# Performance work log

Hardware: AMD Instinct MI355X
Metric: run time of the kernel (lower is better)

## Reference

```python
import jax, jax.numpy as jnp
import numpy as np

B, T, D, P = 8, 2048, 768, 1024


def setup_inputs() -> dict:
    key = jax.random.key(0)
    kx, kp = jax.random.split(key)
    x = jax.random.normal(kx, (B, T, D), dtype=jnp.float32)
    prototypes = jax.random.normal(kp, (P, D), dtype=jnp.float32)
    return {"x": x, "prototypes": prototypes}


def reference(x, prototypes):
    # sum((x[...,None,:] - p)**2, -1) without the [B,T,P,D] intermediate)
    x_sq = jnp.sum(x * x, axis=-1, keepdims=True)          # [B,T,1]
    p_sq = jnp.sum(prototypes * prototypes, axis=-1)        # [P]
    cross = jnp.einsum("btd,pd->btp", x, prototypes)       # [B,T,P]
    distances = x_sq + p_sq[None, None, :] - 2.0 * cross    # [B,T,P]
    return distances, prototypes
```

## Files before the change

kernel.cpp:

```cpp
#include <hip/hip_runtime.h>
#include <hip/hip_bf16.h>
#include <stdint.h>

#define M_ROWS 16384
#define N_COLS 1024
#define K_DIM  768

typedef __attribute__((ext_vector_type(8))) short bf16x8;
typedef __attribute__((ext_vector_type(4))) float f32x4;

__device__ __forceinline__ void async_copy16(void* lds, const void* g) {
  __builtin_amdgcn_global_load_lds(
      (const __attribute__((address_space(1))) unsigned int*)g,
      (__attribute__((address_space(3))) unsigned int*)lds,
      16, 0, 0);
}

__device__ __forceinline__ unsigned short f2bf(float f) {
  __hip_bfloat16 h = __float2bfloat16(f);
  return *reinterpret_cast<unsigned short*>(&h);
}

__global__ void prep_rows(const float* __restrict__ src,
                          unsigned short* __restrict__ dstb,
                          float* __restrict__ sq,
                          float* __restrict__ copy_out) {
  const int wid = threadIdx.x >> 6;
  const int lane = threadIdx.x & 63;
  const int row = blockIdx.x * 4 + wid;
  const float4* r = (const float4*)(src + (size_t)row * K_DIM);
  ushort4* rb = (ushort4*)(dstb + (size_t)row * K_DIM);
  float4* cp = copy_out ? (float4*)(copy_out + (size_t)row * K_DIM) : nullptr;
  float acc = 0.f;
#pragma unroll
  for (int i = 0; i < 3; ++i) {
    float4 v = r[i * 64 + lane];
    acc += v.x * v.x + v.y * v.y + v.z * v.z + v.w * v.w;
    ushort4 u;
    u.x = f2bf(v.x); u.y = f2bf(v.y); u.z = f2bf(v.z); u.w = f2bf(v.w);
    rb[i * 64 + lane] = u;
    if (cp) cp[i * 64 + lane] = v;
  }
#pragma unroll
  for (int off = 32; off; off >>= 1) acc += __shfl_down(acc, off);
  if (lane == 0) sq[row] = acc;
}

__global__ void dist_gemm(const __hip_bfloat16* __restrict__ xb,
                          const __hip_bfloat16* __restrict__ pb,
                          const float* __restrict__ xsq,
                          const float* __restrict__ psq,
                          float* __restrict__ out) {
  __shared__ __hip_bfloat16 As[128 * 32];
  __shared__ __hip_bfloat16 Bs[128 * 32];

  const int flat = blockIdx.x;
  const int xcd = flat & 7;
  const int local = flat >> 3;
  const int bm = xcd * 16 + (local >> 3);
  const int bn = local & 7;

  const int tid = threadIdx.x;
  const int wave = tid >> 6;
  const int lane = tid & 63;
  const int wm = wave >> 1;
  const int wn = wave & 1;

  f32x4 acc[4][4];
#pragma unroll
  for (int i = 0; i < 4; ++i)
#pragma unroll
    for (int j = 0; j < 4; ++j) {
      f32x4 z = {0.f, 0.f, 0.f, 0.f};
      acc[i][j] = z;
    }

  const __hip_bfloat16* Ab = xb + (size_t)(bm * 128) * K_DIM;
  const __hip_bfloat16* Bb = pb + (size_t)(bn * 128) * K_DIM;

  const int sr[2] = {tid >> 2, 64 + (tid >> 2)};
  int gofs[2];
#pragma unroll
  for (int c = 0; c < 2; ++c) {
    const int row = sr[c];
    const int g = (tid & 3) ^ ((row >> 1) & 3);
    gofs[c] = row * K_DIM + g * 8;
  }

  const int rA = lane & 15;
  const int ks = lane >> 4;

  for (int k0 = 0; k0 < K_DIM; k0 += 32) {
#pragma unroll
    for (int c = 0; c < 2; ++c) {
      const int lofs = (c * 256 + tid) * 16;
      async_copy16((char*)As + lofs, Ab + gofs[c] + k0);
      async_copy16((char*)Bs + lofs, Bb + gofs[c] + k0);
    }
    __syncthreads();

    bf16x8 a[4], b[4];
#pragma unroll
    for (int i = 0; i < 4; ++i) {
      const int ra = wm * 64 + i * 16 + rA;
      const int rb = wn * 64 + i * 16 + rA;
      a[i] = *(const bf16x8*)((const char*)As + (ra * 64 + ((ks ^ ((ra >> 1) & 3)) * 16)));
      b[i] = *(const bf16x8*)((const char*)Bs + (rb * 64 + ((ks ^ ((rb >> 1) & 3)) * 16)));
    }
#pragma unroll
    for (int i = 0; i < 4; ++i)
#pragma unroll
      for (int j = 0; j < 4; ++j)
        acc[i][j] = __builtin_amdgcn_mfma_f32_16x16x32_bf16(a[i], b[j], acc[i][j], 0, 0, 0);
    __syncthreads();
  }

  const int colf = lane & 15;
  const int rowg = (lane >> 4) * 4;
#pragma unroll
  for (int j = 0; j < 4; ++j) {
    const int col = bn * 128 + wn * 64 + j * 16 + colf;
    const float ps = psq[col];
#pragma unroll
    for (int i = 0; i < 4; ++i) {
      const int rbase = bm * 128 + wm * 64 + i * 16 + rowg;
#pragma unroll
      for (int r = 0; r < 4; ++r) {
        const int row = rbase + r;
        out[(size_t)row * N_COLS + col] = xsq[row] + ps - 2.0f * acc[i][j][r];
      }
    }
  }
}

extern "C" void kernel_launch(void* const* d_in, const int* in_sizes, int n_in,
                              void* d_out, int out_size, void* d_ws, size_t ws_size,
                              hipStream_t stream) {
  const float* x = (const float*)d_in[0];
  const float* p = (const float*)d_in[1];
  float* out = (float*)d_out;
  char* ws = (char*)d_ws;

  float* xsq = (float*)ws;
  float* psq = (float*)(ws + 65536);
  unsigned short* xb = (unsigned short*)(ws + 69632);
  unsigned short* pb = xb + (size_t)M_ROWS * K_DIM;
  float* proto_out = out + (size_t)M_ROWS * N_COLS;

  prep_rows<<<M_ROWS / 4, 256, 0, stream>>>(x, xb, xsq, nullptr);
  prep_rows<<<N_COLS / 4, 256, 0, stream>>>(p, pb, psq, proto_out);

  dist_gemm<<<1024, 256, 0, stream>>>((const __hip_bfloat16*)xb,
                                      (const __hip_bfloat16*)pb,
                                      xsq, psq, out);
}
```

Baseline: 57.41 us.

## Rewrite distance GEMM as 256x256 double-buffered tile with interleaved prefetch

Replaces the 128x128 single-buffered GEMM, which synchronized twice per 32-wide K step, with 256x256 tiles, 8 waves, 64-wide K steps and double-buffered LDS. Loads for the next K tile are split into four quarter stages interleaved between MFMA clusters, with barriers and setprio to overlap memory and compute. The aim is more operand reuse and hiding global load latency. The cost is 128KB of LDS per block and only 256 blocks, which may underfill the GPU and limit occupancy.

```diff
diff --git a/kernel.cpp b/kernel.cpp
--- a/kernel.cpp
+++ b/kernel.cpp
@@ -5,6 +5,7 @@
 #define M_ROWS 16384
 #define N_COLS 1024
 #define K_DIM  768
+#define NKT    12
 
 typedef __attribute__((ext_vector_type(8))) short bf16x8;
 typedef __attribute__((ext_vector_type(4))) float f32x4;
@@ -46,88 +47,159 @@
   if (lane == 0) sq[row] = acc;
 }
 
-__global__ void dist_gemm(const __hip_bfloat16* __restrict__ xb,
-                          const __hip_bfloat16* __restrict__ pb,
-                          const float* __restrict__ xsq,
-                          const float* __restrict__ psq,
-                          float* __restrict__ out) {
-  __shared__ __hip_bfloat16 As[128 * 32];
-  __shared__ __hip_bfloat16 Bs[128 * 32];
+__device__ __forceinline__ bf16x8 ldsfrag(const char* tile, int row, int slot) {
+  return *(const bf16x8*)(tile + row * 128 + (((slot ^ (row & 7)) << 4)));
+}
+
+__global__ __launch_bounds__(512, 2) void dist_gemm(
+    const __hip_bfloat16* __restrict__ xb,
+    const __hip_bfloat16* __restrict__ pb,
+    const float* __restrict__ xsq,
+    const float* __restrict__ psq,
+    float* __restrict__ out) {
+  __shared__ char lds[2][2][32768];
 
   const int flat = blockIdx.x;
   const int xcd = flat & 7;
   const int local = flat >> 3;
-  const int bm = xcd * 16 + (local >> 3);
-  const int bn = local & 7;
+  const int bm = xcd * 8 + (local >> 2);
+  const int bn = local & 3;
 
   const int tid = threadIdx.x;
   const int wave = tid >> 6;
   const int lane = tid & 63;
-  const int wm = wave >> 1;
-  const int wn = wave & 1;
-
-  f32x4 acc[4][4];
-#pragma unroll
-  for (int i = 0; i < 4; ++i)
-#pragma unroll
-    for (int j = 0; j < 4; ++j) {
-      f32x4 z = {0.f, 0.f, 0.f, 0.f};
-      acc[i][j] = z;
-    }
-
-  const __hip_bfloat16* Ab = xb + (size_t)(bm * 128) * K_DIM;
-  const __hip_bfloat16* Bb = pb + (size_t)(bn * 128) * K_DIM;
-
-  const int sr[2] = {tid >> 2, 64 + (tid >> 2)};
-  int gofs[2];
-#pragma unroll
-  for (int c = 0; c < 2; ++c) {
-    const int row = sr[c];
-    const int g = (tid & 3) ^ ((row >> 1) & 3);
-    gofs[c] = row * K_DIM + g * 8;
-  }
-
-  const int rA = lane & 15;
-  const int ks = lane >> 4;
-
-  for (int k0 = 0; k0 < K_DIM; k0 += 32) {
-#pragma unroll
-    for (int c = 0; c < 2; ++c) {
-      const int lofs = (c * 256 + tid) * 16;
-      async_copy16((char*)As + lofs, Ab + gofs[c] + k0);
-      async_copy16((char*)Bs + lofs, Bb + gofs[c] + k0);
-    }
-    __syncthreads();
-
-    bf16x8 a[4], b[4];
-#pragma unroll
-    for (int i = 0; i < 4; ++i) {
-      const int ra = wm * 64 + i * 16 + rA;
-      const int rb = wn * 64 + i * 16 + rA;
-      a[i] = *(const bf16x8*)((const char*)As + (ra * 64 + ((ks ^ ((ra >> 1) & 3)) * 16)));
-      b[i] = *(const bf16x8*)((const char*)Bs + (rb * 64 + ((ks ^ ((rb >> 1) & 3)) * 16)));
-    }
-#pragma unroll
-    for (int i = 0; i < 4; ++i)
-#pragma unroll
-      for (int j = 0; j < 4; ++j)
-        acc[i][j] = __builtin_amdgcn_mfma_f32_16x16x32_bf16(a[i], b[j], acc[i][j], 0, 0, 0);
-    __syncthreads();
-  }
-
-  const int colf = lane & 15;
-  const int rowg = (lane >> 4) * 4;
-#pragma unroll
-  for (int j = 0; j < 4; ++j) {
-    const int col = bn * 128 + wn * 64 + j * 16 + colf;
-    const float ps = psq[col];
-#pragma unroll
-    for (int i = 0; i < 4; ++i) {
-      const int rbase = bm * 128 + wm * 64 + i * 16 + rowg;
+  const int wm = wave >> 2;
+  const int wn = wave & 3;
+  const int rl = lane & 15;
+  const int kq = lane >> 4;
+
+  f32x4 acc[8][4] = {};
+  bf16x8 af[4][2], bfr[4][2];
+
+  const __hip_bfloat16* Abase = xb + (size_t)(bm * 256) * K_DIM;
+  const __hip_bfloat16* Bbase = pb + (size_t)(bn * 256) * K_DIM;
+
+  const int rih = tid >> 3;
+  const int g8 = (((tid & 7) ^ (rih & 7))) * 8;
+
+#define STAGE(base, tile, h, ktile)                                          \
+  do {                                                                       \
+    _Pragma("unroll") for (int c = 0; c < 2; ++c) {                          \
+      async_copy16((tile) + (h) * 16384 + (c * 512 + tid) * 16,              \
+                   (base) + (size_t)((h) * 128 + c * 64 + rih) * K_DIM +     \
+                       (ktile) * 64 + g8);                                   \
+    }                                                                        \
+  } while (0)
+
+  {
+    char* A0 = &lds[0][0][0];
+    char* B0 = &lds[0][1][0];
+    STAGE(Abase, A0, 0, 0);
+    STAGE(Abase, A0, 1, 0);
+    STAGE(Bbase, B0, 0, 0);
+    STAGE(Bbase, B0, 1, 0);
+  }
+  asm volatile("s_waitcnt vmcnt(0)" ::: "memory");
+  asm volatile("s_barrier" ::: "memory");
+
+  for (int kt = 0; kt < NKT; ++kt) {
+    const char* At = &lds[kt & 1][0][0];
+    const char* Bt = &lds[kt & 1][1][0];
+    char* An = &lds[(kt + 1) & 1][0][0];
+    char* Bn = &lds[(kt + 1) & 1][1][0];
+    const bool pf = (kt + 1 < NKT);
+
+#pragma unroll
+    for (int mi = 0; mi < 4; ++mi)
+#pragma unroll
+      for (int kk = 0; kk < 2; ++kk)
+        af[mi][kk] = ldsfrag(At, wm * 128 + mi * 16 + rl, kk * 4 + kq);
+#pragma unroll
+    for (int ni = 0; ni < 2; ++ni)
+#pragma unroll
+      for (int kk = 0; kk < 2; ++kk)
+        bfr[ni][kk] = ldsfrag(Bt, wn * 64 + ni * 16 + rl, kk * 4 + kq);
+    if (pf) STAGE(Abase, An, 0, kt + 1);
+    asm volatile("s_barrier" ::: "memory");
+    __builtin_amdgcn_s_setprio(1);
+#pragma unroll
+    for (int mi = 0; mi < 4; ++mi)
+#pragma unroll
+      for (int ni = 0; ni < 2; ++ni)
+#pragma unroll
+        for (int kk = 0; kk < 2; ++kk)
+          acc[mi][ni] = __builtin_amdgcn_mfma_f32_16x16x32_bf16(
+              af[mi][kk], bfr[ni][kk], acc[mi][ni], 0, 0, 0);
+    __builtin_amdgcn_s_setprio(0);
+    asm volatile("s_barrier" ::: "memory");
+
+#pragma unroll
+    for (int ni = 2; ni < 4; ++ni)
+#pragma unroll
+      for (int kk = 0; kk < 2; ++kk)
+        bfr[ni][kk] = ldsfrag(Bt, wn * 64 + ni * 16 + rl, kk * 4 + kq);
+    if (pf) STAGE(Abase, An, 1, kt + 1);
+    asm volatile("s_barrier" ::: "memory");
+    __builtin_amdgcn_s_setprio(1);
+#pragma unroll
+    for (int mi = 0; mi < 4; ++mi)
+#pragma unroll
+      for (int ni = 0; ni < 2; ++ni)
+#pragma unroll
+        for (int kk = 0; kk < 2; ++kk)
+          acc[mi][2 + ni] = __builtin_amdgcn_mfma_f32_16x16x32_bf16(
+              af[mi][kk], bfr[2 + ni][kk], acc[mi][2 + ni], 0, 0, 0);
+    __builtin_amdgcn_s_setprio(0);
+    asm volatile("s_barrier" ::: "memory");
+
+#pragma unroll
+    for (int mi = 0; mi < 4; ++mi)
+#pragma unroll
+      for (int kk = 0; kk < 2; ++kk)
+        af[mi][kk] = ldsfrag(At, wm * 128 + 64 + mi * 16 + rl, kk * 4 + kq);
+    if (pf) STAGE(Bbase, Bn, 0, kt + 1);
+    asm volatile("s_barrier" ::: "memory");
+    __builtin_amdgcn_s_setprio(1);
+#pragma unroll
+    for (int mi = 0; mi < 4; ++mi)
+#pragma unroll
+      for (int ni = 0; ni < 2; ++ni)
+#pragma unroll
+        for (int kk = 0; kk < 2; ++kk)
+          acc[4 + mi][ni] = __builtin_amdgcn_mfma_f32_16x16x32_bf16(
+              af[mi][kk], bfr[ni][kk], acc[4 + mi][ni], 0, 0, 0);
+    __builtin_amdgcn_s_setprio(0);
+    asm volatile("s_barrier" ::: "memory");
+
+    if (pf) STAGE(Bbase, Bn, 1, kt + 1);
+    asm volatile("s_barrier" ::: "memory");
+    __builtin_amdgcn_s_setprio(1);
+#pragma unroll
+    for (int mi = 0; mi < 4; ++mi)
+#pragma unroll
+      for (int ni = 0; ni < 2; ++ni)
+#pragma unroll
+        for (int kk = 0; kk < 2; ++kk)
+          acc[4 + mi][2 + ni] = __builtin_amdgcn_mfma_f32_16x16x32_bf16(
+              af[mi][kk], bfr[2 + ni][kk], acc[4 + mi][2 + ni], 0, 0, 0);
+    __builtin_amdgcn_s_setprio(0);
+    asm volatile("s_waitcnt vmcnt(0)" ::: "memory");
+    asm volatile("s_barrier" ::: "memory");
+  }
+#undef STAGE
+
+  const int r0 = bm * 256 + wm * 128;
+  const int c0 = bn * 256 + wn * 64;
+#pragma unroll
+  for (int mf = 0; mf < 8; ++mf) {
+#pragma unroll
+    for (int nf = 0; nf < 4; ++nf) {
+      const int col = c0 + nf * 16 + rl;
+      const float ps = psq[col];
 #pragma unroll
       for (int r = 0; r < 4; ++r) {
-        const int row = rbase + r;
-        out[(size_t)row * N_COLS + col] = xsq[row] + ps - 2.0f * acc[i][j][r];
+        const int row = r0 + mf * 16 + kq * 4 + r;
+        out[(size_t)row * N_COLS + col] = xsq[row] + ps - 2.0f * acc[mf][nf][r];
       }
     }
   }
@@ -150,7 +222,7 @@
   prep_rows<<<M_ROWS / 4, 256, 0, stream>>>(x, xb, xsq, nullptr);
   prep_rows<<<N_COLS / 4, 256, 0, stream>>>(p, pb, psq, proto_out);
 
-  dist_gemm<<<1024, 256, 0, stream>>>((const __hip_bfloat16*)xb,
-                                      (const __hip_bfloat16*)pb,
-                                      xsq, psq, out);
-}
+  dist_gemm<<<256, 512, 0, stream>>>((const __hip_bfloat16*)xb,
+                                     (const __hip_bfloat16*)pb,
+                                     xsq, psq, out);
+}
```

Measured after the change: 51.98 us. 1.1x faster.

## Double-buffer LDS with 64-wide K tiles and merge prep kernels

Applied to the files above, without the earlier changes.

The GEMM now stages 64-wide K tiles into two LDS buffers. The next tile's async global-to-LDS copy is issued before computing on the current one, which replaces the load-sync-compute-sync loop with one barrier per iteration. It uses an 8-way XOR swizzle for the wider rows, raises MFMA wave priority during compute, and sets launch bounds for two blocks per CU. The two prep launches are fused into one kernel to save a launch. LDS use rises to 64KB per block, which may limit occupancy.

```diff
diff --git a/kernel.cpp b/kernel.cpp
--- a/kernel.cpp
+++ b/kernel.cpp
@@ -5,6 +5,7 @@
 #define M_ROWS 16384
 #define N_COLS 1024
 #define K_DIM  768
+#define NKT    12
 
 typedef __attribute__((ext_vector_type(8))) short bf16x8;
 typedef __attribute__((ext_vector_type(4))) float f32x4;
@@ -21,16 +22,31 @@
   return *reinterpret_cast<unsigned short*>(&h);
 }
 
-__global__ void prep_rows(const float* __restrict__ src,
-                          unsigned short* __restrict__ dstb,
-                          float* __restrict__ sq,
-                          float* __restrict__ copy_out) {
+__global__ void prep_all(const float* __restrict__ x,
+                         const float* __restrict__ p,
+                         unsigned short* __restrict__ xb,
+                         unsigned short* __restrict__ pbu,
+                         float* __restrict__ xsq,
+                         float* __restrict__ psq,
+                         float* __restrict__ proto_out) {
+  const int b = blockIdx.x;
   const int wid = threadIdx.x >> 6;
   const int lane = threadIdx.x & 63;
-  const int row = blockIdx.x * 4 + wid;
+  const float* src;
+  unsigned short* dst;
+  float* sq;
+  float* cp;
+  int row;
+  if (b < M_ROWS / 4) {
+    row = b * 4 + wid;
+    src = x; dst = xb; sq = xsq; cp = nullptr;
+  } else {
+    row = (b - M_ROWS / 4) * 4 + wid;
+    src = p; dst = pbu; sq = psq; cp = proto_out;
+  }
   const float4* r = (const float4*)(src + (size_t)row * K_DIM);
-  ushort4* rb = (ushort4*)(dstb + (size_t)row * K_DIM);
-  float4* cp = copy_out ? (float4*)(copy_out + (size_t)row * K_DIM) : nullptr;
+  ushort4* rb = (ushort4*)(dst + (size_t)row * K_DIM);
+  float4* cpv = cp ? (float4*)(cp + (size_t)row * K_DIM) : nullptr;
   float acc = 0.f;
 #pragma unroll
   for (int i = 0; i < 3; ++i) {
@@ -39,20 +55,24 @@
     ushort4 u;
     u.x = f2bf(v.x); u.y = f2bf(v.y); u.z = f2bf(v.z); u.w = f2bf(v.w);
     rb[i * 64 + lane] = u;
-    if (cp) cp[i * 64 + lane] = v;
+    if (cpv) cpv[i * 64 + lane] = v;
   }
 #pragma unroll
   for (int off = 32; off; off >>= 1) acc += __shfl_down(acc, off);
   if (lane == 0) sq[row] = acc;
 }
 
-__global__ void dist_gemm(const __hip_bfloat16* __restrict__ xb,
-                          const __hip_bfloat16* __restrict__ pb,
-                          const float* __restrict__ xsq,
-                          const float* __restrict__ psq,
-                          float* __restrict__ out) {
-  __shared__ __hip_bfloat16 As[128 * 32];
-  __shared__ __hip_bfloat16 Bs[128 * 32];
+__device__ __forceinline__ bf16x8 ldsfrag(const char* tile, int row, int slot) {
+  return *(const bf16x8*)(tile + row * 128 + (((slot ^ (row & 7)) << 4)));
+}
+
+__global__ __launch_bounds__(256, 2) void dist_gemm(
+    const __hip_bfloat16* __restrict__ xb,
+    const __hip_bfloat16* __restrict__ pb,
+    const float* __restrict__ xsq,
+    const float* __restrict__ psq,
+    float* __restrict__ out) {
+  __shared__ char lds[2][2][16384];
 
   const int flat = blockIdx.x;
   const int xcd = flat & 7;
@@ -65,69 +85,81 @@
   const int lane = tid & 63;
   const int wm = wave >> 1;
   const int wn = wave & 1;
+  const int rl = lane & 15;
+  const int kq = lane >> 4;
 
-  f32x4 acc[4][4];
+  f32x4 acc[4][4] = {};
+  bf16x8 af[4][2], bfr[4][2];
+
+  const __hip_bfloat16* Abase = xb + (size_t)(bm * 128) * K_DIM;
+  const __hip_bfloat16* Bbase = pb + (size_t)(bn * 128) * K_DIM;
+
+  int gofs[4];
 #pragma unroll
-  for (int i = 0; i < 4; ++i)
-#pragma unroll
-    for (int j = 0; j < 4; ++j) {
-      f32x4 z = {0.f, 0.f, 0.f, 0.f};
-      acc[i][j] = z;
-    }
-
-  const __hip_bfloat16* Ab = xb + (size_t)(bm * 128) * K_DIM;
-  const __hip_bfloat16* Bb = pb + (size_t)(bn * 128) * K_DIM;
-
-  const int sr[2] = {tid >> 2, 64 + (tid >> 2)};
-  int gofs[2];
-#pragma unroll
-  for (int c = 0; c < 2; ++c) {
-    const int row = sr[c];
-    const int g = (tid & 3) ^ ((row >> 1) & 3);
+  for (int c = 0; c < 4; ++c) {
+    const int row = c * 32 + (tid >> 3);
+    const int g = (tid & 7) ^ (row & 7);
     gofs[c] = row * K_DIM + g * 8;
   }
 
-  const int rA = lane & 15;
-  const int ks = lane >> 4;
+#define STAGE(buf, ktile)                                                   \
+  do {                                                                      \
+    _Pragma("unroll") for (int c = 0; c < 4; ++c) {                         \
+      const int lofs = (c * 256 + tid) * 16;                                \
+      async_copy16(&lds[buf][0][0] + lofs, Abase + gofs[c] + (ktile) * 64); \
+      async_copy16(&lds[buf][1][0] + lofs, Bbase + gofs[c] + (ktile) * 64); \
+    }                                                                       \
+  } while (0)
 
-  for (int k0 = 0; k0 < K_DIM; k0 += 32) {
+  STAGE(0, 0);
+  asm volatile("s_waitcnt vmcnt(0)" ::: "memory");
+  asm volatile("s_barrier" ::: "memory");
+
+  for (int kt = 0; kt < NKT; ++kt) {
+    const int cur = kt & 1;
+    if (kt + 1 < NKT) STAGE(cur ^ 1, kt + 1);
+
+    const char* At = &lds[cur][0][0];
+    const char* Bt = &lds[cur][1][0];
 #pragma unroll
-    for (int c = 0; c < 2; ++c) {
-      const int lofs = (c * 256 + tid) * 16;
-      async_copy16((char*)As + lofs, Ab + gofs[c] + k0);
-      async_copy16((char*)Bs + lofs, Bb + gofs[c] + k0);
-    }
-    __syncthreads();
+    for (int mi = 0; mi < 4; ++mi)
+#pragma unroll
+      for (int kk = 0; kk < 2; ++kk)
+        af[mi][kk] = ldsfrag(At, wm * 64 + mi * 16 + rl, kk * 4 + kq);
+#pragma unroll
+    for (int ni = 0; ni < 4; ++ni)
+#pragma unroll
+      for (int kk = 0; kk < 2; ++kk)
+        bfr[ni][kk] = ldsfrag(Bt, wn * 64 + ni * 16 + rl, kk * 4 + kq);
 
-    bf16x8 a[4], b[4];
+    __builtin_amdgcn_s_setprio(1);
 #pragma unroll
-    for (int i = 0; i < 4; ++i) {
-      const int ra = wm * 64 + i * 16 + rA;
-      const int rb = wn * 64 + i * 16 + rA;
-      a[i] = *(const bf16x8*)((const char*)As + (ra * 64 + ((ks ^ ((ra >> 1) & 3)) * 16)));
-      b[i] = *(const bf16x8*)((const char*)Bs + (rb * 64 + ((ks ^ ((rb >> 1) & 3)) * 16)));
-    }
+    for (int mi = 0; mi < 4; ++mi)
 #pragma unroll
-    for (int i = 0; i < 4; ++i)
+      for (int ni = 0; ni < 4; ++ni)
 #pragma unroll
-      for (int j = 0; j < 4; ++j)
-        acc[i][j] = __builtin_amdgcn_mfma_f32_16x16x32_bf16(a[i], b[j], acc[i][j], 0, 0, 0);
-    __syncthreads();
+        for (int kk = 0; kk < 2; ++kk)
+          acc[mi][ni] = __builtin_amdgcn_mfma_f32_16x16x32_bf16(
+              af[mi][kk], bfr[ni][kk], acc[mi][ni], 0, 0, 0);
+    __builtin_amdgcn_s_setprio(0);
+
+    asm volatile("s_waitcnt vmcnt(0)" ::: "memory");
+    asm volatile("s_barrier" ::: "memory");
   }
+#undef STAGE
 
-  const int colf = lane & 15;
-  const int rowg = (lane >> 4) * 4;
+  const int c0 = bn * 128 + wn * 64;
+  const int r0 = bm * 128 + wm * 64;
 #pragma unroll
-  for (int j = 0; j < 4; ++j) {
-    const int col = bn * 128 + wn * 64 + j * 16 + colf;
-    const float ps = psq[col];
+  for (int mi = 0; mi < 4; ++mi) {
 #pragma unroll
-    for (int i = 0; i < 4; ++i) {
-      const int rbase = bm * 128 + wm * 64 + i * 16 + rowg;
+    for (int ni = 0; ni < 4; ++ni) {
+      const int col = c0 + ni * 16 + rl;
+      const float ps = psq[col];
 #pragma unroll
       for (int r = 0; r < 4; ++r) {
-        const int row = rbase + r;
-        out[(size_t)row * N_COLS + col] = xsq[row] + ps - 2.0f * acc[i][j][r];
+        const int row = r0 + mi * 16 + kq * 4 + r;
+        out[(size_t)row * N_COLS + col] = xsq[row] + ps - 2.0f * acc[mi][ni][r];
       }
     }
   }
@@ -144,13 +176,13 @@
   float* xsq = (float*)ws;
   float* psq = (float*)(ws + 65536);
   unsigned short* xb = (unsigned short*)(ws + 69632);
-  unsigned short* pb = xb + (size_t)M_ROWS * K_DIM;
+  unsigned short* pbu = xb + (size_t)M_ROWS * K_DIM;
   float* proto_out = out + (size_t)M_ROWS * N_COLS;
 
-  prep_rows<<<M_ROWS / 4, 256, 0, stream>>>(x, xb, xsq, nullptr);
-  prep_rows<<<N_COLS / 4, 256, 0, stream>>>(p, pb, psq, proto_out);
+  prep_all<<<M_ROWS / 4 + N_COLS / 4, 256, 0, stream>>>(x, p, xb, pbu, xsq,
+                                                        psq, proto_out);
 
   dist_gemm<<<1024, 256, 0, stream>>>((const __hip_bfloat16*)xb,
-                                      (const __hip_bfloat16*)pb,
+                                      (const __hip_bfloat16*)pbu,
                                       xsq, psq, out);
 }
```

Result: faster. 47.16 us, median of 2 (-17.9%).
